# Kernel tuning notes

Hardware: AMD Instinct MI355X
Metric: run time of the kernel (lower is better)

Reference implementation:

```python
import jax, jax.numpy as jnp
import numpy as np

N_NODES = 100000
DIM_IN = 128
DIM_H = 64
LATENT = 64
N_EDGES = 1200000


def setup_inputs() -> dict:
    key = jax.random.key(0)
    ks = jax.random.split(key, 8)
    x = jax.random.normal(ks[0], (N_NODES, DIM_IN), dtype=jnp.float32)
    edge_index = jax.random.randint(ks[1], (2, N_EDGES), 0, N_NODES, dtype=jnp.int32)
    batch = jnp.zeros((N_NODES,), dtype=jnp.int32)
    s_in = 1.0 / np.sqrt(DIM_IN)
    s_h = 1.0 / np.sqrt(DIM_H)
    gcn_w = jax.random.uniform(ks[2], (DIM_IN, DIM_H), jnp.float32, -s_in, s_in)
    gcn_b = jnp.zeros((DIM_H,), dtype=jnp.float32)
    w1 = jax.random.uniform(ks[3], (DIM_H, LATENT), jnp.float32, -s_h, s_h)
    b1 = jax.random.uniform(ks[4], (LATENT,), jnp.float32, -s_h, s_h)
    s_l = 1.0 / np.sqrt(LATENT)
    w3 = jax.random.uniform(ks[5], (LATENT, LATENT), jnp.float32, -s_l, s_l)
    b3 = jax.random.uniform(ks[6], (LATENT,), jnp.float32, -s_l, s_l)
    return {"x": x, "edge_index": edge_index, "batch": batch,
            "gcn_w": gcn_w, "gcn_b": gcn_b, "w1": w1, "b1": b1, "w3": w3, "b3": b3}


def _gcn_conv(x, edge_index, W, b):
    n = x.shape[0]
    loop = jnp.arange(n, dtype=edge_index.dtype)
    src = jnp.concatenate([edge_index[0], loop])
    dst = jnp.concatenate([edge_index[1], loop])
    deg = jax.ops.segment_sum(jnp.ones_like(dst, dtype=x.dtype), dst, num_segments=n)
    dinv = jnp.where(deg > 0, jax.lax.rsqrt(deg), 0.0)
    norm = dinv[src] * dinv[dst]                      # [E+N]
    h = x @ W                                          # [N, dim_h]
    msg = h[src] * norm[:, None]                       # gather + scale
    out = jax.ops.segment_sum(msg, dst, num_segments=n)  # scatter-add
    return out + b


def reference(x, edge_index, batch, gcn_w, gcn_b, w1, b1, w3, b3):
    g1 = _gcn_conv(x, edge_index, gcn_w, gcn_b)
    l1 = g1 @ w1 + b1
    l3 = l1 @ w3 + b3
    # mu/sigma/z/kl in the original are side effects not returned; output is l3
    return l3
```

## Files before the change

kernel.cpp:

```cpp
#include <hip/hip_runtime.h>
#include <hip/hip_bf16.h>

#define N_NODES 100000
#define N_EDGES 1200000
#define NBK 256
#define NPB 391
#define CAPB 5376
#define EPB 4096
#define BIN_BLKS 293
#define XW_BLKS 1280
#define FUSED_GRID (BIN_BLKS + XW_BLKS)

typedef __attribute__((ext_vector_type(8))) short bf16x8;
typedef __attribute__((ext_vector_type(4))) float f32x4;

__global__ __launch_bounds__(256) void k_w1(const float* __restrict__ w1,
                                            const float* __restrict__ w3,
                                            const float* __restrict__ gcn_b,
                                            const float* __restrict__ b1,
                                            float* __restrict__ tmp,
                                            float* __restrict__ tb) {
    const int i = blockIdx.x * 256 + threadIdx.x;
    const int r = i >> 6, c = i & 63;
    float a = 0.f;
#pragma unroll 8
    for (int k = 0; k < 64; ++k) a = fmaf(w1[r * 64 + k], w3[k * 64 + c], a);
    tmp[i] = a;
    if (blockIdx.x == 0 && threadIdx.x < 64) {
        const int t = threadIdx.x;
        float s = b1[t];
        for (int k = 0; k < 64; ++k) s = fmaf(gcn_b[k], w1[k * 64 + t], s);
        tb[t] = s;
    }
}

__global__ __launch_bounds__(256) void k_w2(const float* __restrict__ gcn_w,
                                            const float* __restrict__ tmp,
                                            const float* __restrict__ tb,
                                            const float* __restrict__ w3,
                                            const float* __restrict__ b3,
                                            short* __restrict__ WcB,
                                            float* __restrict__ bc) {
    const int i = blockIdx.x * 256 + threadIdx.x;
    const int r = i >> 6, c = i & 63;
    float a = 0.f;
#pragma unroll 8
    for (int k = 0; k < 64; ++k) a = fmaf(gcn_w[r * 64 + k], tmp[k * 64 + c], a);
    const int kt = r >> 5, kr = r & 31, g = kr >> 3, e = kr & 7;
    const int ct = c & 3, cl = c >> 2, lane = g * 16 + cl;
    WcB[(((kt * 4 + ct) * 64) + lane) * 8 + e] =
        __builtin_bit_cast(short, __float2bfloat16(a));
    if (blockIdx.x == 0 && threadIdx.x < 64) {
        const int t = threadIdx.x;
        float s = b3[t];
        for (int k = 0; k < 64; ++k) s = fmaf(tb[k], w3[k * 64 + t], s);
        bc[t] = s;
    }
}

__global__ __launch_bounds__(256) void k_fused(const int* __restrict__ ei,
                                               int* __restrict__ bcnt,
                                               int* __restrict__ binned,
                                               const float* __restrict__ x,
                                               const short* __restrict__ WcB,
                                               unsigned char* __restrict__ hsq,
                                               float* __restrict__ hscale) {
    const int b = blockIdx.x;
    if (b < BIN_BLKS) {
        __shared__ int hist[NBK], base[NBK], cur[NBK];
        const int t = threadIdx.x;
        const int e0 = b * EPB;
        for (int i = t; i < NBK; i += 256) hist[i] = 0;
        __syncthreads();
        for (int j = t; j < EPB; j += 256) {
            const int e = e0 + j;
            if (e < N_EDGES) atomicAdd(&hist[ei[N_EDGES + e] / NPB], 1);
        }
        __syncthreads();
        for (int i = t; i < NBK; i += 256) {
            const int h = hist[i];
            base[i] = h ? atomicAdd(&bcnt[i], h) : 0;
            cur[i] = 0;
        }
        __syncthreads();
        for (int j = t; j < EPB; j += 256) {
            const int e = e0 + j;
            if (e < N_EDGES) {
                const int s = ei[e];
                const int d = ei[N_EDGES + e];
                const int bk = d / NPB;
                const int dl = d - bk * NPB;
                const int p = base[bk] + atomicAdd(&cur[bk], 1);
                if (p < CAPB) binned[bk * CAPB + p] = s | (dl << 17);
            }
        }
    } else {
        const int t = threadIdx.x, w = t >> 6, lane = t & 63;
        const int cl = lane & 15, g = lane >> 4;
        bf16x8 bfrag[16];
#pragma unroll
        for (int f = 0; f < 16; ++f) bfrag[f] = ((const bf16x8*)WcB)[f * 64 + lane];

        const int ntiles = N_NODES / 16;
        const int nw = XW_BLKS * 4;
        for (int tile = (b - BIN_BLKS) * 4 + w; tile < ntiles; tile += nw) {
            const int node0 = tile * 16;
            const float* xrow = x + (size_t)(node0 + cl) * 128 + g * 8;
            f32x4 xa[4][2];
#pragma unroll
            for (int kt = 0; kt < 4; ++kt) {
                xa[kt][0] = *(const f32x4*)(xrow + kt * 32);
                xa[kt][1] = *(const f32x4*)(xrow + kt * 32 + 4);
            }
            f32x4 acc[4];
#pragma unroll
            for (int ct = 0; ct < 4; ++ct) acc[ct] = (f32x4){0.f, 0.f, 0.f, 0.f};
#pragma unroll
            for (int kt = 0; kt < 4; ++kt) {
                bf16x8 af;
#pragma unroll
                for (int j = 0; j < 4; ++j) {
                    af[j]     = __builtin_bit_cast(short, __float2bfloat16(xa[kt][0][j]));
                    af[j + 4] = __builtin_bit_cast(short, __float2bfloat16(xa[kt][1][j]));
                }
#pragma unroll
                for (int ct = 0; ct < 4; ++ct)
                    acc[ct] = __builtin_amdgcn_mfma_f32_16x16x32_bf16(
                        af, bfrag[kt * 4 + ct], acc[ct], 0, 0, 0);
            }
            float mx[4];
#pragma unroll
            for (int j = 0; j < 4; ++j) {
                mx[j] = fmaxf(fmaxf(fabsf(acc[0][j]), fabsf(acc[1][j])),
                              fmaxf(fabsf(acc[2][j]), fabsf(acc[3][j])));
            }
#pragma unroll
            for (int m = 1; m < 16; m <<= 1)
#pragma unroll
                for (int j = 0; j < 4; ++j)
                    mx[j] = fmaxf(mx[j], __shfl_xor(mx[j], m));
#pragma unroll
            for (int j = 0; j < 4; ++j) {
                const float sc = fmaxf(mx[j], 1e-20f) * (1.f / 127.f);
                const float inv = 127.f / fmaxf(mx[j], 1e-20f);
                unsigned int pk = 0;
#pragma unroll
                for (int ct = 0; ct < 4; ++ct) {
                    const int v = (int)rintf(acc[ct][j] * inv) + 128;
                    pk |= (unsigned int)v << (8 * ct);
                }
                *(unsigned int*)(hsq + (size_t)(node0 + g * 4 + j) * 64 + cl * 4) = pk;
                if (cl == j) hscale[node0 + g * 4 + j] = sc;
            }
        }
    }
}

__global__ __launch_bounds__(512) void k_csr(const int* __restrict__ bcnt,
                                             const int* __restrict__ binned,
                                             const float* __restrict__ hscale,
                                             int* __restrict__ csr,
                                             int* __restrict__ rowptr,
                                             int* __restrict__ degA,
                                             float* __restrict__ dinv,
                                             float* __restrict__ csca) {
    __shared__ int stage[CAPB];
    __shared__ int sdeg[NPB], sloc[NPB], scur[NPB];
    const int b = blockIdx.x, t = threadIdx.x;
    const int m = min(bcnt[b], CAPB);
    for (int i = t; i < NPB; i += 512) { sdeg[i] = 0; scur[i] = 0; }
    __syncthreads();
    for (int j = t; j < m; j += 512) {
        const int pk = binned[b * CAPB + j];
        stage[j] = pk;
        atomicAdd(&sdeg[pk >> 17], 1);
    }
    __syncthreads();
    if (t < 64) {
        int run = 0;
#pragma unroll
        for (int c0 = 0; c0 < NPB; c0 += 64) {
            const int idx = c0 + t;
            const int v = (idx < NPB) ? sdeg[idx] : 0;
            int inc = v;
#pragma unroll
            for (int o = 1; o < 64; o <<= 1) {
                const int u = __shfl_up(inc, o);
                if (t >= o) inc += u;
            }
            if (idx < NPB) sloc[idx] = run + inc - v;
            run += __shfl(inc, 63);
        }
    }
    __syncthreads();
    for (int i = t; i < NPB; i += 512) {
        const int node = b * NPB + i;
        if (node < N_NODES) {
            const int v = sdeg[i];
            const float dv = rsqrtf((float)(v + 1));
            rowptr[node] = b * CAPB + sloc[i];
            degA[node] = v;
            dinv[node] = dv;
            csca[node] = dv * hscale[node];
        }
    }
    for (int j = t; j < m; j += 512) {
        const int pk = stage[j];
        const int dl = pk >> 17;
        const int p = atomicAdd(&scur[dl], 1);
        csr[b * CAPB + sloc[dl] + p] = pk & 0x1FFFF;
    }
}

__global__ __launch_bounds__(256) void k_gather(const int* __restrict__ rowptr,
                                                const int* __restrict__ degA,
                                                const int* __restrict__ csr,
                                                const unsigned char* __restrict__ hsq,
                                                const float* __restrict__ csca,
                                                const float* __restrict__ dinv,
                                                const float* __restrict__ bc,
                                                float* __restrict__ out) {
    const int t = threadIdx.x, wave = t >> 6, lane = t & 63;
    const int node = blockIdx.x * 4 + wave;
    if (node >= N_NODES) return;
    const int deg = degA[node];
    const int base = rowptr[node];
    const float dvn = dinv[node];
    const int cl = lane & 15, g = lane >> 4;
    const int cc = cl * 4;

    f32x4 acc = (f32x4){0.f, 0.f, 0.f, 0.f};
    float T = 0.f;
    for (int j0 = 0; j0 < deg; j0 += 64) {
        const int rem = min(deg - j0, 64);
        int s_l = 0;
        float c_l = 0.f;
        if (lane < rem) {
            s_l = csr[base + j0 + lane];
            c_l = csca[s_l];
        }
        for (int i0 = 0; i0 < rem; i0 += 16) {
#pragma unroll
            for (int u = 0; u < 4; ++u) {
                const int jj = i0 + u * 4 + g;
                const int sj = __shfl(s_l, jj);
                const float cj = __shfl(c_l, jj);
                if (jj < rem) {
                    const unsigned int q =
                        *(const unsigned int*)(hsq + (size_t)sj * 64 + cc);
                    acc[0] = fmaf((float)(q & 0xFFu), cj, acc[0]);
                    acc[1] = fmaf((float)((q >> 8) & 0xFFu), cj, acc[1]);
                    acc[2] = fmaf((float)((q >> 16) & 0xFFu), cj, acc[2]);
                    acc[3] = fmaf((float)(q >> 24), cj, acc[3]);
                    T += cj;
                }
            }
        }
    }
#pragma unroll
    for (int k = 0; k < 4; ++k) {
        acc[k] = fmaf(-128.f, T, acc[k]);
        acc[k] += __shfl_xor(acc[k], 16);
        acc[k] += __shfl_xor(acc[k], 32);
    }
    const unsigned int qs = *(const unsigned int*)(hsq + (size_t)node * 64 + cc);
    const float cs = csca[node];
    const float4 bc4 = *(const float4*)(bc + cc);
    float4 res;
    res.x = fmaf(fmaf(((float)(qs & 0xFFu)) - 128.f, cs, acc[0]), dvn, bc4.x);
    res.y = fmaf(fmaf(((float)((qs >> 8) & 0xFFu)) - 128.f, cs, acc[1]), dvn, bc4.y);
    res.z = fmaf(fmaf(((float)((qs >> 16) & 0xFFu)) - 128.f, cs, acc[2]), dvn, bc4.z);
    res.w = fmaf(fmaf(((float)(qs >> 24)) - 128.f, cs, acc[3]), dvn, bc4.w);
    if (g == 0) *(float4*)(out + (size_t)node * 64 + cc) = res;
}

extern "C" void kernel_launch(void* const* d_in, const int* in_sizes, int n_in,
                              void* d_out, int out_size, void* d_ws, size_t ws_size,
                              hipStream_t stream) {
    const float* x     = (const float*)d_in[0];
    const int*   ei    = (const int*)d_in[1];
    const float* gcn_w = (const float*)d_in[3];
    const float* gcn_b = (const float*)d_in[4];
    const float* w1    = (const float*)d_in[5];
    const float* b1    = (const float*)d_in[6];
    const float* w3    = (const float*)d_in[7];
    const float* b3    = (const float*)d_in[8];
    float* out = (float*)d_out;

    char* ws = (char*)d_ws;
    int*           bcnt   = (int*)(ws);
    short*         WcB    = (short*)(ws + 1024);
    float*         bc     = (float*)(ws + 17408);
    float*         tmp    = (float*)(ws + 17664);
    float*         tb     = (float*)(ws + 34048);
    float*         dinv   = (float*)(ws + 34304);
    int*           rowptr = (int*)(ws + 434304);
    int*           degA   = (int*)(ws + 834304);
    float*         hscale = (float*)(ws + 1234304);
    float*         csca   = (float*)(ws + 1634304);
    unsigned char* hsq    = (unsigned char*)(ws + 2034304);
    int*           binned = (int*)(ws + 8434304);
    int*           csr    = (int*)(ws + 13939328);

    hipMemsetAsync(bcnt, 0, NBK * sizeof(int), stream);
    k_w1<<<16, 256, 0, stream>>>(w1, w3, gcn_b, b1, tmp, tb);
    k_w2<<<32, 256, 0, stream>>>(gcn_w, tmp, tb, w3, b3, WcB, bc);
    k_fused<<<FUSED_GRID, 256, 0, stream>>>(ei, bcnt, binned, x, WcB, hsq, hscale);
    k_csr<<<NBK, 512, 0, stream>>>(bcnt, binned, hscale, csr, rowptr, degA, dinv, csca);
    k_gather<<<(N_NODES + 3) / 4, 256, 0, stream>>>(rowptr, degA, csr, hsq, csca,
                                                    dinv, bc, out);
}
```

Baseline: 105.2 us.

## Pack per-edge source scale into CSR entries and switch to signed int8 quantization

Adds a degree pass (k_deg2) so that k_csr can fold a 15-bit truncated float of each source's scale into the upper bits of every CSR entry. The gather kernel then skips the dependent random load of csca per edge. Quantized features become signed int8, which removes the +128 offset bookkeeping. The two weight-precompute kernels and the memset are merged into one kernel that recomputes w1@w3 in shared memory in every block. The cost is an extra kernel launch and pass over the binned edges, the redundant weight product per block, and a small precision loss in the per-edge scale.

```diff
diff --git a/kernel.cpp b/kernel.cpp
--- a/kernel.cpp
+++ b/kernel.cpp
@@ -14,34 +14,33 @@
 typedef __attribute__((ext_vector_type(8))) short bf16x8;
 typedef __attribute__((ext_vector_type(4))) float f32x4;
 
-__global__ __launch_bounds__(256) void k_w1(const float* __restrict__ w1,
-                                            const float* __restrict__ w3,
-                                            const float* __restrict__ gcn_b,
-                                            const float* __restrict__ b1,
-                                            float* __restrict__ tmp,
-                                            float* __restrict__ tb) {
-    const int i = blockIdx.x * 256 + threadIdx.x;
-    const int r = i >> 6, c = i & 63;
-    float a = 0.f;
-#pragma unroll 8
-    for (int k = 0; k < 64; ++k) a = fmaf(w1[r * 64 + k], w3[k * 64 + c], a);
-    tmp[i] = a;
-    if (blockIdx.x == 0 && threadIdx.x < 64) {
-        const int t = threadIdx.x;
+__global__ __launch_bounds__(256) void k_w(const float* __restrict__ gcn_w,
+                                           const float* __restrict__ gcn_b,
+                                           const float* __restrict__ w1,
+                                           const float* __restrict__ b1,
+                                           const float* __restrict__ w3,
+                                           const float* __restrict__ b3,
+                                           short* __restrict__ WcB,
+                                           float* __restrict__ bc,
+                                           int* __restrict__ bcnt) {
+    __shared__ float tmp[4096];
+    __shared__ float tb[64];
+    const int b = blockIdx.x, t = threadIdx.x;
+    if (b == 31 && t < NBK) bcnt[t] = 0;
+    if (b == 0 && t < 64) {
         float s = b1[t];
         for (int k = 0; k < 64; ++k) s = fmaf(gcn_b[k], w1[k * 64 + t], s);
         tb[t] = s;
     }
-}
-
-__global__ __launch_bounds__(256) void k_w2(const float* __restrict__ gcn_w,
-                                            const float* __restrict__ tmp,
-                                            const float* __restrict__ tb,
-                                            const float* __restrict__ w3,
-                                            const float* __restrict__ b3,
-                                            short* __restrict__ WcB,
-                                            float* __restrict__ bc) {
-    const int i = blockIdx.x * 256 + threadIdx.x;
+    for (int i = t; i < 4096; i += 256) {
+        const int r = i >> 6, c = i & 63;
+        float a = 0.f;
+#pragma unroll 8
+        for (int k = 0; k < 64; ++k) a = fmaf(w1[r * 64 + k], w3[k * 64 + c], a);
+        tmp[i] = a;
+    }
+    __syncthreads();
+    const int i = b * 256 + t;
     const int r = i >> 6, c = i & 63;
     float a = 0.f;
 #pragma unroll 8
@@ -50,8 +49,7 @@
     const int ct = c & 3, cl = c >> 2, lane = g * 16 + cl;
     WcB[(((kt * 4 + ct) * 64) + lane) * 8 + e] =
         __builtin_bit_cast(short, __float2bfloat16(a));
-    if (blockIdx.x == 0 && threadIdx.x < 64) {
-        const int t = threadIdx.x;
+    if (b == 0 && t < 64) {
         float s = b3[t];
         for (int k = 0; k < 64; ++k) s = fmaf(tb[k], w3[k * 64 + t], s);
         bc[t] = s;
@@ -146,8 +144,8 @@
                 unsigned int pk = 0;
 #pragma unroll
                 for (int ct = 0; ct < 4; ++ct) {
-                    const int v = (int)rintf(acc[ct][j] * inv) + 128;
-                    pk |= (unsigned int)v << (8 * ct);
+                    const int v = (int)rintf(acc[ct][j] * inv);
+                    pk |= ((unsigned int)(v & 0xFF)) << (8 * ct);
                 }
                 *(unsigned int*)(hsq + (size_t)(node0 + g * 4 + j) * 64 + cl * 4) = pk;
                 if (cl == j) hscale[node0 + g * 4 + j] = sc;
@@ -156,25 +154,48 @@
     }
 }
 
+__global__ __launch_bounds__(256) void k_deg2(const int* __restrict__ bcnt,
+                                              const int* __restrict__ binned,
+                                              const float* __restrict__ hscale,
+                                              int* __restrict__ degA,
+                                              float* __restrict__ dinv,
+                                              float* __restrict__ csca) {
+    __shared__ int ldeg[NPB];
+    const int b = blockIdx.x, t = threadIdx.x;
+    for (int i = t; i < NPB; i += 256) ldeg[i] = 0;
+    __syncthreads();
+    const int m = min(bcnt[b], CAPB);
+    for (int j = t; j < m; j += 256)
+        atomicAdd(&ldeg[binned[b * CAPB + j] >> 17], 1);
+    __syncthreads();
+    for (int i = t; i < NPB; i += 256) {
+        const int node = b * NPB + i;
+        if (node < N_NODES) {
+            const int v = ldeg[i];
+            const float dv = rsqrtf((float)(v + 1));
+            degA[node] = v;
+            dinv[node] = dv;
+            csca[node] = dv * hscale[node];
+        }
+    }
+}
+
 __global__ __launch_bounds__(512) void k_csr(const int* __restrict__ bcnt,
                                              const int* __restrict__ binned,
-                                             const float* __restrict__ hscale,
+                                             const int* __restrict__ degA,
+                                             const float* __restrict__ csca,
                                              int* __restrict__ csr,
-                                             int* __restrict__ rowptr,
-                                             int* __restrict__ degA,
-                                             float* __restrict__ dinv,
-                                             float* __restrict__ csca) {
+                                             int* __restrict__ rowptr) {
     __shared__ int stage[CAPB];
     __shared__ int sdeg[NPB], sloc[NPB], scur[NPB];
     const int b = blockIdx.x, t = threadIdx.x;
     const int m = min(bcnt[b], CAPB);
-    for (int i = t; i < NPB; i += 512) { sdeg[i] = 0; scur[i] = 0; }
-    __syncthreads();
-    for (int j = t; j < m; j += 512) {
-        const int pk = binned[b * CAPB + j];
-        stage[j] = pk;
-        atomicAdd(&sdeg[pk >> 17], 1);
-    }
+    for (int i = t; i < NPB; i += 512) {
+        const int node = b * NPB + i;
+        sdeg[i] = (node < N_NODES) ? degA[node] : 0;
+        scur[i] = 0;
+    }
+    for (int j = t; j < m; j += 512) stage[j] = binned[b * CAPB + j];
     __syncthreads();
     if (t < 64) {
         int run = 0;
@@ -195,20 +216,16 @@
     __syncthreads();
     for (int i = t; i < NPB; i += 512) {
         const int node = b * NPB + i;
-        if (node < N_NODES) {
-            const int v = sdeg[i];
-            const float dv = rsqrtf((float)(v + 1));
-            rowptr[node] = b * CAPB + sloc[i];
-            degA[node] = v;
-            dinv[node] = dv;
-            csca[node] = dv * hscale[node];
-        }
+        if (node < N_NODES) rowptr[node] = b * CAPB + sloc[i];
     }
     for (int j = t; j < m; j += 512) {
         const int pk = stage[j];
         const int dl = pk >> 17;
+        const int s = pk & 0x1FFFF;
+        const unsigned cu = __float_as_uint(csca[s]);
+        const unsigned c15 = ((cu + 0x8000u) >> 16) & 0x7FFFu;
         const int p = atomicAdd(&scur[dl], 1);
-        csr[b * CAPB + sloc[dl] + p] = pk & 0x1FFFF;
+        csr[b * CAPB + sloc[dl] + p] = s | (int)(c15 << 17);
     }
 }
 
@@ -226,51 +243,45 @@
     const int deg = degA[node];
     const int base = rowptr[node];
     const float dvn = dinv[node];
+    const float csN = csca[node];
     const int cl = lane & 15, g = lane >> 4;
     const int cc = cl * 4;
+    const unsigned int qs = *(const unsigned int*)(hsq + (size_t)node * 64 + cc);
 
     f32x4 acc = (f32x4){0.f, 0.f, 0.f, 0.f};
-    float T = 0.f;
     for (int j0 = 0; j0 < deg; j0 += 64) {
         const int rem = min(deg - j0, 64);
-        int s_l = 0;
-        float c_l = 0.f;
-        if (lane < rem) {
-            s_l = csr[base + j0 + lane];
-            c_l = csca[s_l];
-        }
+        int e_l = 0;
+        if (lane < rem) e_l = csr[base + j0 + lane];
         for (int i0 = 0; i0 < rem; i0 += 16) {
 #pragma unroll
             for (int u = 0; u < 4; ++u) {
                 const int jj = i0 + u * 4 + g;
-                const int sj = __shfl(s_l, jj);
-                const float cj = __shfl(c_l, jj);
+                const int ej = __shfl(e_l, jj);
                 if (jj < rem) {
+                    const int sj = ej & 0x1FFFF;
+                    const float cj = __uint_as_float(((unsigned)ej >> 17) << 16);
                     const unsigned int q =
                         *(const unsigned int*)(hsq + (size_t)sj * 64 + cc);
-                    acc[0] = fmaf((float)(q & 0xFFu), cj, acc[0]);
-                    acc[1] = fmaf((float)((q >> 8) & 0xFFu), cj, acc[1]);
-                    acc[2] = fmaf((float)((q >> 16) & 0xFFu), cj, acc[2]);
-                    acc[3] = fmaf((float)(q >> 24), cj, acc[3]);
-                    T += cj;
+                    acc[0] = fmaf((float)(int)(signed char)(q & 0xFFu), cj, acc[0]);
+                    acc[1] = fmaf((float)(int)(signed char)((q >> 8) & 0xFFu), cj, acc[1]);
+                    acc[2] = fmaf((float)(int)(signed char)((q >> 16) & 0xFFu), cj, acc[2]);
+                    acc[3] = fmaf((float)(int)(signed char)(q >> 24), cj, acc[3]);
                 }
             }
         }
     }
 #pragma unroll
     for (int k = 0; k < 4; ++k) {
-        acc[k] = fmaf(-128.f, T, acc[k]);
         acc[k] += __shfl_xor(acc[k], 16);
         acc[k] += __shfl_xor(acc[k], 32);
     }
-    const unsigned int qs = *(const unsigned int*)(hsq + (size_t)node * 64 + cc);
-    const float cs = csca[node];
     const float4 bc4 = *(const float4*)(bc + cc);
     float4 res;
-    res.x = fmaf(fmaf(((float)(qs & 0xFFu)) - 128.f, cs, acc[0]), dvn, bc4.x);
-    res.y = fmaf(fmaf(((float)((qs >> 8) & 0xFFu)) - 128.f, cs, acc[1]), dvn, bc4.y);
-    res.z = fmaf(fmaf(((float)((qs >> 16) & 0xFFu)) - 128.f, cs, acc[2]), dvn, bc4.z);
-    res.w = fmaf(fmaf(((float)(qs >> 24)) - 128.f, cs, acc[3]), dvn, bc4.w);
+    res.x = fmaf(fmaf((float)(int)(signed char)(qs & 0xFFu), csN, acc[0]), dvn, bc4.x);
+    res.y = fmaf(fmaf((float)(int)(signed char)((qs >> 8) & 0xFFu), csN, acc[1]), dvn, bc4.y);
+    res.z = fmaf(fmaf((float)(int)(signed char)((qs >> 16) & 0xFFu), csN, acc[2]), dvn, bc4.z);
+    res.w = fmaf(fmaf((float)(int)(signed char)(qs >> 24), csN, acc[3]), dvn, bc4.w);
     if (g == 0) *(float4*)(out + (size_t)node * 64 + cc) = res;
 }
 
@@ -291,22 +302,19 @@
     int*           bcnt   = (int*)(ws);
     short*         WcB    = (short*)(ws + 1024);
     float*         bc     = (float*)(ws + 17408);
-    float*         tmp    = (float*)(ws + 17664);
-    float*         tb     = (float*)(ws + 34048);
-    float*         dinv   = (float*)(ws + 34304);
-    int*           rowptr = (int*)(ws + 434304);
-    int*           degA   = (int*)(ws + 834304);
-    float*         hscale = (float*)(ws + 1234304);
-    float*         csca   = (float*)(ws + 1634304);
-    unsigned char* hsq    = (unsigned char*)(ws + 2034304);
-    int*           binned = (int*)(ws + 8434304);
-    int*           csr    = (int*)(ws + 13939328);
-
-    hipMemsetAsync(bcnt, 0, NBK * sizeof(int), stream);
-    k_w1<<<16, 256, 0, stream>>>(w1, w3, gcn_b, b1, tmp, tb);
-    k_w2<<<32, 256, 0, stream>>>(gcn_w, tmp, tb, w3, b3, WcB, bc);
+    float*         dinv   = (float*)(ws + 17664);
+    int*           rowptr = (int*)(ws + 417664);
+    int*           degA   = (int*)(ws + 817664);
+    float*         hscale = (float*)(ws + 1217664);
+    float*         csca   = (float*)(ws + 1617664);
+    unsigned char* hsq    = (unsigned char*)(ws + 2017664);
+    int*           binned = (int*)(ws + 8417664);
+    int*           csr    = (int*)(ws + 13922688);
+
+    k_w<<<32, 256, 0, stream>>>(gcn_w, gcn_b, w1, b1, w3, b3, WcB, bc, bcnt);
     k_fused<<<FUSED_GRID, 256, 0, stream>>>(ei, bcnt, binned, x, WcB, hsq, hscale);
-    k_csr<<<NBK, 512, 0, stream>>>(bcnt, binned, hscale, csr, rowptr, degA, dinv, csca);
+    k_deg2<<<NBK, 256, 0, stream>>>(bcnt, binned, hscale, degA, dinv, csca);
+    k_csr<<<NBK, 512, 0, stream>>>(bcnt, binned, degA, csca, csr, rowptr);
     k_gather<<<(N_NODES + 3) / 4, 256, 0, stream>>>(rowptr, degA, csr, hsq, csca,
                                                     dinv, bc, out);
 }
```

Result: slower. 120.3 us (+14.4%).
